# Kernel optimization log

Hardware: AMD Instinct MI355X
Metric: run time of the kernel (lower is better)

Reference implementation:

```python
import jax, jax.numpy as jnp
import numpy as np

B, S, DM, H = 2, 4096, 512, 8
DEPTH = DM // H


def setup_inputs() -> dict:
    key = jax.random.key(0)
    ks = jax.random.split(key, 12)
    scale = 1.0 / np.sqrt(DM)
    return {
        "q": jax.random.normal(ks[0], (B, S, DM), jnp.float32),
        "k": jax.random.normal(ks[1], (B, S, DM), jnp.float32),
        "v": jax.random.normal(ks[2], (B, S, DM), jnp.float32),
        # padding-style mask: 1.0 = masked position, 0.0 = attend
        "mask": jax.random.bernoulli(ks[3], 0.1, (B, 1, 1, S)).astype(jnp.float32),
        "Wq": jax.random.normal(ks[4], (DM, DM), jnp.float32) * scale,
        "bq": jnp.zeros((DM,), jnp.float32),
        "Wk": jax.random.normal(ks[5], (DM, DM), jnp.float32) * scale,
        "bk": jnp.zeros((DM,), jnp.float32),
        "Wv": jax.random.normal(ks[6], (DM, DM), jnp.float32) * scale,
        "bv": jnp.zeros((DM,), jnp.float32),
        "Wo": jax.random.normal(ks[7], (DM, DM), jnp.float32) * scale,
        "bo": jnp.zeros((DM,), jnp.float32),
    }


def _split_heads(x):
    # [B, S, DM] -> [B, H, S, DEPTH]
    b, s, _ = x.shape
    return x.reshape(b, s, H, DEPTH).transpose(0, 2, 1, 3)


def reference(q, k, v, mask, Wq, bq, Wk, bk, Wv, bv, Wo, bo):
    qh = _split_heads(q @ Wq + bq)   # [B,H,S,D]
    kh = _split_heads(k @ Wk + bk)
    vh = _split_heads(v @ Wv + bv)
    logits = jnp.einsum("bhqd,bhkd->bhqk", qh, kh) / jnp.sqrt(
        jnp.asarray(DEPTH, qh.dtype))
    logits = logits + mask * (-1e9)
    attn = jax.nn.softmax(logits, axis=-1)          # [B,H,Sq,Sk]
    out = jnp.einsum("bhqk,bhkd->bhqd", attn, vh)   # [B,H,S,D]
    out = out.transpose(0, 2, 1, 3).reshape(q.shape[0], -1, DM)
    return out @ Wo + bo
```

## Files before the change

### kernel.cpp

```cpp
#include <hip/hip_runtime.h>
#include <math.h>

#define BDIM 2
#define SDIM 4096
#define DMODEL 512
#define NHEAD 8
#define DHEAD 64
#define MROWS (BDIM * SDIM)

typedef __attribute__((ext_vector_type(8))) short short8;
typedef __attribute__((ext_vector_type(4))) float f32x4;

#define MFMA16(a, b, c) __builtin_amdgcn_mfma_f32_16x16x32_bf16((a), (b), (c), 0, 0, 0)
#define EXP2F(x) __builtin_amdgcn_exp2f(x)

#define SCALE2 0.18033688011112042f
#define MASKMUL -1.442695040e9f
#define M0C 16.0f

__device__ inline void bf16_split(float x, short& h, short& l) {
  unsigned u = __float_as_uint(x);
  h = (short)(u >> 16);
  float hf = __uint_as_float(u & 0xffff0000u);
  l = (short)(__float_as_uint(x - hf) >> 16);
}

__global__ __launch_bounds__(256) void wsplit_kernel(
    const float* __restrict__ W0, const float* __restrict__ W1,
    const float* __restrict__ W2, const float* __restrict__ W3,
    short* __restrict__ T0h, short* __restrict__ T0l, short* __restrict__ T1h,
    short* __restrict__ T1l, short* __restrict__ T2h, short* __restrict__ T2l,
    short* __restrict__ T3h, short* __restrict__ T3l) {
  __shared__ short Th[64 * 72], Tl[64 * 72];
  const int tid = threadIdx.x;
  const int k0 = blockIdx.x * 64;
  const int n0 = blockIdx.y * 64;
  const int z = blockIdx.z;
  const float* W = (z == 0) ? W0 : (z == 1) ? W1 : (z == 2) ? W2 : W3;
  short* Oh = (z == 0) ? T0h : (z == 1) ? T1h : (z == 2) ? T2h : T3h;
  short* Ol = (z == 0) ? T0l : (z == 1) ? T1l : (z == 2) ? T2l : T3l;

  {
    const int r = tid >> 2;
    const int c16 = (tid & 3) * 16;
    short8 h0, h1, l0, l1;
#pragma unroll
    for (int g = 0; g < 2; g++) {
      const f32x4 a = *(const f32x4*)(W + (size_t)(k0 + r) * DMODEL + n0 + c16 + g * 8);
      const f32x4 b = *(const f32x4*)(W + (size_t)(k0 + r) * DMODEL + n0 + c16 + g * 8 + 4);
      short8& hh = g ? h1 : h0;
      short8& ll = g ? l1 : l0;
#pragma unroll
      for (int j = 0; j < 4; j++) {
        short x, y;
        bf16_split(a[j], x, y);
        hh[j] = x;
        ll[j] = y;
        bf16_split(b[j], x, y);
        hh[4 + j] = x;
        ll[4 + j] = y;
      }
    }
    *(short8*)&Th[r * 72 + c16] = h0;
    *(short8*)&Th[r * 72 + c16 + 8] = h1;
    *(short8*)&Tl[r * 72 + c16] = l0;
    *(short8*)&Tl[r * 72 + c16 + 8] = l1;
  }
  __syncthreads();
  {
    const int n = tid >> 2;
    const int kc = (tid & 3) * 16;
    short8 h0, h1, l0, l1;
#pragma unroll
    for (int i = 0; i < 8; i++) {
      h0[i] = Th[(kc + i) * 72 + n];
      h1[i] = Th[(kc + 8 + i) * 72 + n];
      l0[i] = Tl[(kc + i) * 72 + n];
      l1[i] = Tl[(kc + 8 + i) * 72 + n];
    }
    short* dh = Oh + (size_t)(n0 + n) * DMODEL + k0 + kc;
    short* dl = Ol + (size_t)(n0 + n) * DMODEL + k0 + kc;
    *(short8*)dh = h0;
    *(short8*)(dh + 8) = h1;
    *(short8*)dl = l0;
    *(short8*)(dl + 8) = l1;
  }
}

template <int MODE>
__global__ __launch_bounds__(256, 4) void proj_mfma_kernel(
    const float* __restrict__ X, const short* __restrict__ Wth,
    const short* __restrict__ Wtl, const float* __restrict__ bias,
    float* __restrict__ out, short* __restrict__ oh, short* __restrict__ ol) {
  __shared__ short Xh[64 * 72], Xl[64 * 72];
  __shared__ short Wh[64 * 72], Wl[64 * 72];

  const int tid = threadIdx.x;
  const int lane = tid & 63;
  const int w = tid >> 6;
  const int lane15 = lane & 15;
  const int quad = lane >> 4;
  const int wm = (w >> 1) * 32;
  const int wn = (w & 1) * 32;
  const int m0 = blockIdx.x * 64;
  const int n0 = blockIdx.y * 64;

  f32x4 c[2][2];
#pragma unroll
  for (int mt = 0; mt < 2; mt++)
#pragma unroll
    for (int nt = 0; nt < 2; nt++) c[mt][nt] = (f32x4){0.f, 0.f, 0.f, 0.f};

  const int sr = tid >> 2;
  const int sc16 = (tid & 3) * 16;

  for (int k0 = 0; k0 < DMODEL; k0 += 64) {
    {
      short8 h0, h1, l0, l1;
#pragma unroll
      for (int g = 0; g < 2; g++) {
        const f32x4 a =
            *(const f32x4*)(X + (size_t)(m0 + sr) * DMODEL + k0 + sc16 + g * 8);
        const f32x4 b = *(const f32x4*)(X + (size_t)(m0 + sr) * DMODEL + k0 +
                                        sc16 + g * 8 + 4);
        short8& hh = g ? h1 : h0;
        short8& ll = g ? l1 : l0;
#pragma unroll
        for (int j = 0; j < 4; j++) {
          short x, y;
          bf16_split(a[j], x, y);
          hh[j] = x;
          ll[j] = y;
          bf16_split(b[j], x, y);
          hh[4 + j] = x;
          ll[4 + j] = y;
        }
      }
      *(short8*)&Xh[sr * 72 + sc16] = h0;
      *(short8*)&Xh[sr * 72 + sc16 + 8] = h1;
      *(short8*)&Xl[sr * 72 + sc16] = l0;
      *(short8*)&Xl[sr * 72 + sc16 + 8] = l1;

      const short* wsh = Wth + (size_t)(n0 + sr) * DMODEL + k0 + sc16;
      const short* wsl = Wtl + (size_t)(n0 + sr) * DMODEL + k0 + sc16;
      *(short8*)&Wh[sr * 72 + sc16] = *(const short8*)wsh;
      *(short8*)&Wh[sr * 72 + sc16 + 8] = *(const short8*)(wsh + 8);
      *(short8*)&Wl[sr * 72 + sc16] = *(const short8*)wsl;
      *(short8*)&Wl[sr * 72 + sc16 + 8] = *(const short8*)(wsl + 8);
    }
    __syncthreads();

#pragma unroll
    for (int ks = 0; ks < 2; ks++) {
      short8 ah[2], al[2], bh[2], bl[2];
#pragma unroll
      for (int mt = 0; mt < 2; mt++) {
        const int xo = (wm + mt * 16 + lane15) * 72 + ks * 32 + quad * 8;
        ah[mt] = *(const short8*)&Xh[xo];
        al[mt] = *(const short8*)&Xl[xo];
      }
#pragma unroll
      for (int nt = 0; nt < 2; nt++) {
        const int wo = (wn + nt * 16 + lane15) * 72 + ks * 32 + quad * 8;
        bh[nt] = *(const short8*)&Wh[wo];
        bl[nt] = *(const short8*)&Wl[wo];
      }
#pragma unroll
      for (int mt = 0; mt < 2; mt++)
#pragma unroll
        for (int nt = 0; nt < 2; nt++) {
          c[mt][nt] = MFMA16(ah[mt], bh[nt], c[mt][nt]);
          c[mt][nt] = MFMA16(ah[mt], bl[nt], c[mt][nt]);
          c[mt][nt] = MFMA16(al[mt], bh[nt], c[mt][nt]);
        }
    }
    __syncthreads();
  }

#pragma unroll
  for (int nt = 0; nt < 2; nt++) {
    const int n = n0 + wn + nt * 16 + lane15;
    const float bb = bias[n];
#pragma unroll
    for (int mt = 0; mt < 2; mt++)
#pragma unroll
      for (int r = 0; r < 4; r++) {
        const int m = m0 + wm + mt * 16 + quad * 4 + r;
        const float val = c[mt][nt][r] + bb;
        if (MODE == 1) {
          const int bidx = m >> 12;
          const int s = m & 4095;
          const int hh = n >> 6;
          const int d = n & 63;
          const size_t off =
              ((size_t)(bidx * NHEAD + hh) * SDIM + s) * DHEAD + d;
          short x, y;
          bf16_split(val, x, y);
          oh[off] = x;
          ol[off] = y;
        } else {
          out[(size_t)m * DMODEL + n] = val;
        }
      }
  }
}

__global__ __launch_bounds__(256) void vtrans_kernel(
    const short* __restrict__ vh, const short* __restrict__ vl,
    short* __restrict__ vth, short* __restrict__ vtl) {
  __shared__ short Th[64 * 72], Tl[64 * 72];
  const int tid = threadIdx.x;
  const int s0 = blockIdx.x * 64;
  const int h = blockIdx.y;
  const int b = blockIdx.z;
  const size_t base = (size_t)(b * NHEAD + h) * SDIM * DHEAD;

  {
    const int s = tid >> 2;
    const int c = tid & 3;
    const short* srcH = vh + base + (size_t)(s0 + s) * DHEAD + c * 16;
    const short* srcL = vl + base + (size_t)(s0 + s) * DHEAD + c * 16;
    *(short8*)&Th[s * 72 + c * 16] = *(const short8*)srcH;
    *(short8*)&Th[s * 72 + c * 16 + 8] = *(const short8*)(srcH + 8);
    *(short8*)&Tl[s * 72 + c * 16] = *(const short8*)srcL;
    *(short8*)&Tl[s * 72 + c * 16 + 8] = *(const short8*)(srcL + 8);
  }
  __syncthreads();
  {
    const int d = tid & 63;
    const int cw = tid >> 6;
    short8 a0, a1, b0, b1;
#pragma unroll
    for (int i = 0; i < 8; i++) {
      a0[i] = Th[(cw * 16 + i) * 72 + d];
      a1[i] = Th[(cw * 16 + 8 + i) * 72 + d];
      b0[i] = Tl[(cw * 16 + i) * 72 + d];
      b1[i] = Tl[(cw * 16 + 8 + i) * 72 + d];
    }
    short* dstH = vth + base + (size_t)d * SDIM + s0 + cw * 16;
    short* dstL = vtl + base + (size_t)d * SDIM + s0 + cw * 16;
    *(short8*)dstH = a0;
    *(short8*)(dstH + 8) = a1;
    *(short8*)dstL = b0;
    *(short8*)(dstL + 8) = b1;
  }
}

#define KP 72
#define VP 72
#define PP 68

__global__ __launch_bounds__(256, 2) void flash_attn_kernel(
    const short* __restrict__ qhh, const short* __restrict__ qhl,
    const short* __restrict__ khh, const short* __restrict__ khl,
    const short* __restrict__ vth, const short* __restrict__ vtl,
    const float* __restrict__ mask, float* __restrict__ ctx) {
  __shared__ short Ksh[64 * KP], Ksl[64 * KP];
  __shared__ short Vsh[64 * VP], Vsl[64 * VP];
  __shared__ float Ps[128 * PP];

  const int tid = threadIdx.x;
  const int lane = tid & 63;
  const int w = tid >> 6;
  const int lane15 = lane & 15;
  const int quad = lane >> 4;
  const int q0 = blockIdx.x * 128;
  const int h = blockIdx.y;
  const int b = blockIdx.z;

  const size_t base = (size_t)(b * NHEAD + h) * SDIM * DHEAD;
  const short* Qh = qhh + base;
  const short* Ql = qhl + base;
  const short* Kh = khh + base;
  const short* Kl = khl + base;
  const short* Vh = vth + base;
  const short* Vl = vtl + base;
  const float* mb = mask + (size_t)b * SDIM;

  short8 qfh[2][2], qfl[2][2];
#pragma unroll
  for (int mt = 0; mt < 2; mt++) {
    const size_t row = q0 + w * 32 + mt * 16 + lane15;
#pragma unroll
    for (int ks = 0; ks < 2; ks++) {
      qfh[mt][ks] = *(const short8*)(Qh + row * DHEAD + ks * 32 + quad * 8);
      qfl[mt][ks] = *(const short8*)(Ql + row * DHEAD + ks * 32 + quad * 8);
    }
  }

  f32x4 o[2][4];
#pragma unroll
  for (int mt = 0; mt < 2; mt++)
#pragma unroll
    for (int dt = 0; dt < 4; dt++) o[mt][dt] = (f32x4){0.f, 0.f, 0.f, 0.f};
  float lr[2][4];
#pragma unroll
  for (int mt = 0; mt < 2; mt++)
#pragma unroll
    for (int r = 0; r < 4; r++) lr[mt][r] = 0.f;

  short8 onesb;
#pragma unroll
  for (int j = 0; j < 8; j++) onesb[j] = (short)0x3F80;

  const int sr = tid >> 2;
  const int sc = (tid & 3) * 16;

  for (int kt = 0; kt < SDIM / 64; kt++) {
    const int k0 = kt * 64;
    {
      const short8 a0 = *(const short8*)(Kh + (size_t)(k0 + sr) * DHEAD + sc);
      const short8 a1 = *(const short8*)(Kh + (size_t)(k0 + sr) * DHEAD + sc + 8);
      const short8 b0 = *(const short8*)(Kl + (size_t)(k0 + sr) * DHEAD + sc);
      const short8 b1 = *(const short8*)(Kl + (size_t)(k0 + sr) * DHEAD + sc + 8);
      const short8 c0 = *(const short8*)(Vh + (size_t)sr * SDIM + k0 + sc);
      const short8 c1 = *(const short8*)(Vh + (size_t)sr * SDIM + k0 + sc + 8);
      const short8 d0 = *(const short8*)(Vl + (size_t)sr * SDIM + k0 + sc);
      const short8 d1 = *(const short8*)(Vl + (size_t)sr * SDIM + k0 + sc + 8);
      *(short8*)&Ksh[sr * KP + sc] = a0;
      *(short8*)&Ksh[sr * KP + sc + 8] = a1;
      *(short8*)&Ksl[sr * KP + sc] = b0;
      *(short8*)&Ksl[sr * KP + sc + 8] = b1;
      *(short8*)&Vsh[sr * VP + sc] = c0;
      *(short8*)&Vsh[sr * VP + sc + 8] = c1;
      *(short8*)&Vsl[sr * VP + sc] = d0;
      *(short8*)&Vsl[sr * VP + sc + 8] = d1;
    }
    float mv[4];
#pragma unroll
    for (int nt = 0; nt < 4; nt++)
      mv[nt] = fmaf(mb[k0 + nt * 16 + lane15], MASKMUL, -M0C);
    __syncthreads();

#pragma unroll
    for (int mt = 0; mt < 2; mt++)
#pragma unroll
      for (int nt = 0; nt < 4; nt++) {
        f32x4 acc = (f32x4){0.f, 0.f, 0.f, 0.f};
#pragma unroll
        for (int ks = 0; ks < 2; ks++) {
          const int koff = (nt * 16 + lane15) * KP + ks * 32 + quad * 8;
          const short8 kbh = *(const short8*)&Ksh[koff];
          const short8 kbl = *(const short8*)&Ksl[koff];
          acc = MFMA16(qfh[mt][ks], kbh, acc);
          acc = MFMA16(qfh[mt][ks], kbl, acc);
          acc = MFMA16(qfl[mt][ks], kbh, acc);
        }
#pragma unroll
        for (int r = 0; r < 4; r++) {
          const float p = EXP2F(fmaf(acc[r], SCALE2, mv[nt]));
          Ps[(w * 32 + mt * 16 + quad * 4 + r) * PP + nt * 16 + lane15] = p;
        }
      }

    short8 pah[2][2], pal[2][2];
#pragma unroll
    for (int mt = 0; mt < 2; mt++)
#pragma unroll
      for (int kf = 0; kf < 2; kf++) {
        const float* pr =
            &Ps[(w * 32 + mt * 16 + lane15) * PP + kf * 32 + quad * 8];
        const f32x4 p0 = *(const f32x4*)pr;
        const f32x4 p1 = *(const f32x4*)(pr + 4);
        short8 ph, pl;
#pragma unroll
        for (int j = 0; j < 4; j++) {
          short hh, ll;
          bf16_split(p0[j], hh, ll);
          ph[j] = hh;
          pl[j] = ll;
        }
#pragma unroll
        for (int j = 0; j < 4; j++) {
          short hh, ll;
          bf16_split(p1[j], hh, ll);
          ph[4 + j] = hh;
          pl[4 + j] = ll;
        }
        pah[mt][kf] = ph;
        pal[mt][kf] = pl;
      }

#pragma unroll
    for (int mt = 0; mt < 2; mt++) {
      f32x4 racc = (f32x4){0.f, 0.f, 0.f, 0.f};
#pragma unroll
      for (int kf = 0; kf < 2; kf++) {
        racc = MFMA16(pah[mt][kf], onesb, racc);
        racc = MFMA16(pal[mt][kf], onesb, racc);
      }
#pragma unroll
      for (int r = 0; r < 4; r++) lr[mt][r] += racc[r];
    }

#pragma unroll
    for (int dt = 0; dt < 4; dt++)
#pragma unroll
      for (int kf = 0; kf < 2; kf++) {
        const int voff = (dt * 16 + lane15) * VP + kf * 32 + quad * 8;
        const short8 vbh = *(const short8*)&Vsh[voff];
        const short8 vbl = *(const short8*)&Vsl[voff];
#pragma unroll
        for (int mt = 0; mt < 2; mt++) {
          o[mt][dt] = MFMA16(pah[mt][kf], vbh, o[mt][dt]);
          o[mt][dt] = MFMA16(pah[mt][kf], vbl, o[mt][dt]);
          o[mt][dt] = MFMA16(pal[mt][kf], vbh, o[mt][dt]);
        }
      }
    __syncthreads();
  }

  float inv[2][4];
#pragma unroll
  for (int mt = 0; mt < 2; mt++)
#pragma unroll
    for (int r = 0; r < 4; r++) inv[mt][r] = 1.f / lr[mt][r];
#pragma unroll
  for (int mt = 0; mt < 2; mt++)
#pragma unroll
    for (int dt = 0; dt < 4; dt++)
#pragma unroll
      for (int r = 0; r < 4; r++) {
        const int q = q0 + w * 32 + mt * 16 + quad * 4 + r;
        const int col = h * DHEAD + dt * 16 + lane15;
        ctx[((size_t)b * SDIM + q) * DMODEL + col] = o[mt][dt][r] * inv[mt][r];
      }
}

extern "C" void kernel_launch(void* const* d_in, const int* in_sizes, int n_in,
                              void* d_out, int out_size, void* d_ws,
                              size_t ws_size, hipStream_t stream) {
  const float* q = (const float*)d_in[0];
  const float* k = (const float*)d_in[1];
  const float* v = (const float*)d_in[2];
  const float* mask = (const float*)d_in[3];
  const float* Wq = (const float*)d_in[4];
  const float* bq = (const float*)d_in[5];
  const float* Wk = (const float*)d_in[6];
  const float* bk = (const float*)d_in[7];
  const float* Wv = (const float*)d_in[8];
  const float* bv = (const float*)d_in[9];
  const float* Wo = (const float*)d_in[10];
  const float* bo = (const float*)d_in[11];
  float* out = (float*)d_out;

  char* W = (char*)d_ws;
  const size_t SZB = (size_t)MROWS * DMODEL * sizeof(short);
  short* q_h = (short*)(W + 0 * SZB);
  short* q_l = (short*)(W + 1 * SZB);
  short* k_h = (short*)(W + 2 * SZB);
  short* k_l = (short*)(W + 3 * SZB);
  short* v_h = (short*)(W + 4 * SZB);
  short* v_l = (short*)(W + 5 * SZB);
  short* vt_h = (short*)(W + 6 * SZB);
  short* vt_l = (short*)(W + 7 * SZB);
  float* ctx = (float*)(W + 4 * SZB);
  const size_t WSZ = (size_t)DMODEL * DMODEL * sizeof(short);
  char* WT = W + 8 * SZB;
  short* wtq_h = (short*)(WT + 0 * WSZ);
  short* wtq_l = (short*)(WT + 1 * WSZ);
  short* wtk_h = (short*)(WT + 2 * WSZ);
  short* wtk_l = (short*)(WT + 3 * WSZ);
  short* wtv_h = (short*)(WT + 4 * WSZ);
  short* wtv_l = (short*)(WT + 5 * WSZ);
  short* wto_h = (short*)(WT + 6 * WSZ);
  short* wto_l = (short*)(WT + 7 * WSZ);

  wsplit_kernel<<<dim3(DMODEL / 64, DMODEL / 64, 4), 256, 0, stream>>>(
      Wq, Wk, Wv, Wo, wtq_h, wtq_l, wtk_h, wtk_l, wtv_h, wtv_l, wto_h, wto_l);

  const dim3 gproj(MROWS / 64, DMODEL / 64);
  proj_mfma_kernel<1><<<gproj, 256, 0, stream>>>(q, wtq_h, wtq_l, bq, nullptr,
                                                 q_h, q_l);
  proj_mfma_kernel<1><<<gproj, 256, 0, stream>>>(k, wtk_h, wtk_l, bk, nullptr,
                                                 k_h, k_l);
  proj_mfma_kernel<1><<<gproj, 256, 0, stream>>>(v, wtv_h, wtv_l, bv, nullptr,
                                                 v_h, v_l);

  vtrans_kernel<<<dim3(SDIM / 64, NHEAD, BDIM), 256, 0, stream>>>(v_h, v_l,
                                                                  vt_h, vt_l);

  flash_attn_kernel<<<dim3(SDIM / 128, NHEAD, BDIM), 256, 0, stream>>>(
      q_h, q_l, k_h, k_l, vt_h, vt_l, mask, ctx);

  proj_mfma_kernel<0><<<gproj, 256, 0, stream>>>(ctx, wto_h, wto_l, bo, out,
                                                 nullptr, nullptr);
}
```

Measured before the change: 424.5 us.

## Pre-split activations, double-buffer projection GEMM with LDS DMA, prefetch K/V in attention

```diff
diff --git a/kernel.cpp b/kernel.cpp
--- a/kernel.cpp
+++ b/kernel.cpp
@@ -17,6 +17,11 @@
 #define SCALE2 0.18033688011112042f
 #define MASKMUL -1.442695040e9f
 #define M0C 16.0f
+
+#define GLOAD_LDS16(g, l)                                                     \
+  __builtin_amdgcn_global_load_lds(                                           \
+      (const __attribute__((address_space(1))) void*)(g),                     \
+      (__attribute__((address_space(3))) void*)(l), 16, 0, 0)
 
 __device__ inline void bf16_split(float x, short& h, short& l) {
   unsigned u = __float_as_uint(x);
@@ -87,98 +92,110 @@
   }
 }
 
+__global__ __launch_bounds__(256) void xsplit_kernel(const float* __restrict__ X,
+                                                     short* __restrict__ Xh,
+                                                     short* __restrict__ Xl) {
+  const size_t i = ((size_t)blockIdx.x * 256 + threadIdx.x) * 8;
+  const f32x4 a = *(const f32x4*)(X + i);
+  const f32x4 b = *(const f32x4*)(X + i + 4);
+  short8 h, l;
+#pragma unroll
+  for (int j = 0; j < 4; j++) {
+    short x, y;
+    bf16_split(a[j], x, y);
+    h[j] = x;
+    l[j] = y;
+    bf16_split(b[j], x, y);
+    h[4 + j] = x;
+    l[4 + j] = y;
+  }
+  *(short8*)(Xh + i) = h;
+  *(short8*)(Xl + i) = l;
+}
+
 template <int MODE>
-__global__ __launch_bounds__(256, 4) void proj_mfma_kernel(
-    const float* __restrict__ X, const short* __restrict__ Wth,
-    const short* __restrict__ Wtl, const float* __restrict__ bias,
-    float* __restrict__ out, short* __restrict__ oh, short* __restrict__ ol) {
-  __shared__ short Xh[64 * 72], Xl[64 * 72];
-  __shared__ short Wh[64 * 72], Wl[64 * 72];
-
+__global__ __launch_bounds__(512, 2) void proj2_kernel(
+    const short* __restrict__ Xh, const short* __restrict__ Xl,
+    const short* __restrict__ Wth, const short* __restrict__ Wtl,
+    const float* __restrict__ bias, float* __restrict__ out,
+    short* __restrict__ oh, short* __restrict__ ol) {
+  __shared__ short L[2 * 20480];
   const int tid = threadIdx.x;
   const int lane = tid & 63;
   const int w = tid >> 6;
   const int lane15 = lane & 15;
   const int quad = lane >> 4;
-  const int wm = (w >> 1) * 32;
-  const int wn = (w & 1) * 32;
   const int m0 = blockIdx.x * 64;
-  const int n0 = blockIdx.y * 64;
-
-  f32x4 c[2][2];
+  const int n0 = blockIdx.y * 256;
+  const int wm = (w >> 2) * 32;
+  const int wn = (w & 3) * 64;
+
+  const short* gp[5];
+  int ldso[5];
+#pragma unroll
+  for (int i = 0; i < 5; i++) {
+    const int idx = w * 5 + i;
+    const int g = idx * 64 + lane;
+    if (g < 512) {
+      const short* src = (g < 256) ? Xh : Xl;
+      const int a = g & 255;
+      gp[i] = src + (size_t)(m0 + (a >> 2)) * DMODEL + (a & 3) * 8;
+    } else {
+      const int gg = g - 512;
+      const short* src = (gg < 1024) ? Wth : Wtl;
+      const int a = gg & 1023;
+      gp[i] = src + (size_t)(n0 + (a >> 2)) * DMODEL + (a & 3) * 8;
+    }
+    ldso[i] = idx * 512;
+  }
+
+  f32x4 c[2][4];
 #pragma unroll
   for (int mt = 0; mt < 2; mt++)
 #pragma unroll
-    for (int nt = 0; nt < 2; nt++) c[mt][nt] = (f32x4){0.f, 0.f, 0.f, 0.f};
-
-  const int sr = tid >> 2;
-  const int sc16 = (tid & 3) * 16;
-
-  for (int k0 = 0; k0 < DMODEL; k0 += 64) {
-    {
-      short8 h0, h1, l0, l1;
-#pragma unroll
-      for (int g = 0; g < 2; g++) {
-        const f32x4 a =
-            *(const f32x4*)(X + (size_t)(m0 + sr) * DMODEL + k0 + sc16 + g * 8);
-        const f32x4 b = *(const f32x4*)(X + (size_t)(m0 + sr) * DMODEL + k0 +
-                                        sc16 + g * 8 + 4);
-        short8& hh = g ? h1 : h0;
-        short8& ll = g ? l1 : l0;
-#pragma unroll
-        for (int j = 0; j < 4; j++) {
-          short x, y;
-          bf16_split(a[j], x, y);
-          hh[j] = x;
-          ll[j] = y;
-          bf16_split(b[j], x, y);
-          hh[4 + j] = x;
-          ll[4 + j] = y;
-        }
-      }
-      *(short8*)&Xh[sr * 72 + sc16] = h0;
-      *(short8*)&Xh[sr * 72 + sc16 + 8] = h1;
-      *(short8*)&Xl[sr * 72 + sc16] = l0;
-      *(short8*)&Xl[sr * 72 + sc16 + 8] = l1;
-
-      const short* wsh = Wth + (size_t)(n0 + sr) * DMODEL + k0 + sc16;
-      const short* wsl = Wtl + (size_t)(n0 + sr) * DMODEL + k0 + sc16;
-      *(short8*)&Wh[sr * 72 + sc16] = *(const short8*)wsh;
-      *(short8*)&Wh[sr * 72 + sc16 + 8] = *(const short8*)(wsh + 8);
-      *(short8*)&Wl[sr * 72 + sc16] = *(const short8*)wsl;
-      *(short8*)&Wl[sr * 72 + sc16 + 8] = *(const short8*)(wsl + 8);
-    }
+    for (int nt = 0; nt < 4; nt++) c[mt][nt] = (f32x4){0.f, 0.f, 0.f, 0.f};
+
+  constexpr int NT = DMODEL / 32;
+
+#pragma unroll
+  for (int i = 0; i < 5; i++) GLOAD_LDS16(gp[i], &L[ldso[i]]);
+
+  for (int t = 0; t < NT; t++) {
     __syncthreads();
-
-#pragma unroll
-    for (int ks = 0; ks < 2; ks++) {
-      short8 ah[2], al[2], bh[2], bl[2];
-#pragma unroll
-      for (int mt = 0; mt < 2; mt++) {
-        const int xo = (wm + mt * 16 + lane15) * 72 + ks * 32 + quad * 8;
-        ah[mt] = *(const short8*)&Xh[xo];
-        al[mt] = *(const short8*)&Xl[xo];
-      }
-#pragma unroll
-      for (int nt = 0; nt < 2; nt++) {
-        const int wo = (wn + nt * 16 + lane15) * 72 + ks * 32 + quad * 8;
-        bh[nt] = *(const short8*)&Wh[wo];
-        bl[nt] = *(const short8*)&Wl[wo];
-      }
-#pragma unroll
-      for (int mt = 0; mt < 2; mt++)
-#pragma unroll
-        for (int nt = 0; nt < 2; nt++) {
-          c[mt][nt] = MFMA16(ah[mt], bh[nt], c[mt][nt]);
-          c[mt][nt] = MFMA16(ah[mt], bl[nt], c[mt][nt]);
-          c[mt][nt] = MFMA16(al[mt], bh[nt], c[mt][nt]);
-        }
-    }
-    __syncthreads();
-  }
-
-#pragma unroll
-  for (int nt = 0; nt < 2; nt++) {
+    if (t + 1 < NT) {
+      short* dst = &L[((t + 1) & 1) * 20480];
+#pragma unroll
+      for (int i = 0; i < 5; i++)
+        GLOAD_LDS16(gp[i] + (t + 1) * 32, dst + ldso[i]);
+    }
+    const short* buf = &L[(t & 1) * 20480];
+    short8 ah[2], al[2], bh[4], bl[4];
+#pragma unroll
+    for (int mt = 0; mt < 2; mt++) {
+      const int r = wm + mt * 16 + lane15;
+      ah[mt] = *(const short8*)&buf[r * 32 + quad * 8];
+      al[mt] = *(const short8*)&buf[2048 + r * 32 + quad * 8];
+    }
+#pragma unroll
+    for (int nt = 0; nt < 4; nt++) {
+      const int r = wn + nt * 16 + lane15;
+      bh[nt] = *(const short8*)&buf[4096 + r * 32 + quad * 8];
+      bl[nt] = *(const short8*)&buf[12288 + r * 32 + quad * 8];
+    }
+    __builtin_amdgcn_s_setprio(1);
+#pragma unroll
+    for (int mt = 0; mt < 2; mt++)
+#pragma unroll
+      for (int nt = 0; nt < 4; nt++) {
+        c[mt][nt] = MFMA16(ah[mt], bh[nt], c[mt][nt]);
+        c[mt][nt] = MFMA16(ah[mt], bl[nt], c[mt][nt]);
+        c[mt][nt] = MFMA16(al[mt], bh[nt], c[mt][nt]);
+      }
+    __builtin_amdgcn_s_setprio(0);
+  }
+
+#pragma unroll
+  for (int nt = 0; nt < 4; nt++) {
     const int n = n0 + wn + nt * 16 + lane15;
     const float bb = bias[n];
 #pragma unroll
@@ -254,7 +271,8 @@
     const short* __restrict__ qhh, const short* __restrict__ qhl,
     const short* __restrict__ khh, const short* __restrict__ khl,
     const short* __restrict__ vth, const short* __restrict__ vtl,
-    const float* __restrict__ mask, float* __restrict__ ctx) {
+    const float* __restrict__ mask, short* __restrict__ ctxh,
+    short* __restrict__ ctxl) {
   __shared__ short Ksh[64 * KP], Ksl[64 * KP];
   __shared__ short Vsh[64 * VP], Vsl[64 * VP];
   __shared__ float Ps[128 * PP];
@@ -306,32 +324,48 @@
   const int sr = tid >> 2;
   const int sc = (tid & 3) * 16;
 
+  short8 rg[8];
+  rg[0] = *(const short8*)(Kh + (size_t)sr * DHEAD + sc);
+  rg[1] = *(const short8*)(Kh + (size_t)sr * DHEAD + sc + 8);
+  rg[2] = *(const short8*)(Kl + (size_t)sr * DHEAD + sc);
+  rg[3] = *(const short8*)(Kl + (size_t)sr * DHEAD + sc + 8);
+  rg[4] = *(const short8*)(Vh + (size_t)sr * SDIM + sc);
+  rg[5] = *(const short8*)(Vh + (size_t)sr * SDIM + sc + 8);
+  rg[6] = *(const short8*)(Vl + (size_t)sr * SDIM + sc);
+  rg[7] = *(const short8*)(Vl + (size_t)sr * SDIM + sc + 8);
+
   for (int kt = 0; kt < SDIM / 64; kt++) {
     const int k0 = kt * 64;
-    {
-      const short8 a0 = *(const short8*)(Kh + (size_t)(k0 + sr) * DHEAD + sc);
-      const short8 a1 = *(const short8*)(Kh + (size_t)(k0 + sr) * DHEAD + sc + 8);
-      const short8 b0 = *(const short8*)(Kl + (size_t)(k0 + sr) * DHEAD + sc);
-      const short8 b1 = *(const short8*)(Kl + (size_t)(k0 + sr) * DHEAD + sc + 8);
-      const short8 c0 = *(const short8*)(Vh + (size_t)sr * SDIM + k0 + sc);
-      const short8 c1 = *(const short8*)(Vh + (size_t)sr * SDIM + k0 + sc + 8);
-      const short8 d0 = *(const short8*)(Vl + (size_t)sr * SDIM + k0 + sc);
-      const short8 d1 = *(const short8*)(Vl + (size_t)sr * SDIM + k0 + sc + 8);
-      *(short8*)&Ksh[sr * KP + sc] = a0;
-      *(short8*)&Ksh[sr * KP + sc + 8] = a1;
-      *(short8*)&Ksl[sr * KP + sc] = b0;
-      *(short8*)&Ksl[sr * KP + sc + 8] = b1;
-      *(short8*)&Vsh[sr * VP + sc] = c0;
-      *(short8*)&Vsh[sr * VP + sc + 8] = c1;
-      *(short8*)&Vsl[sr * VP + sc] = d0;
-      *(short8*)&Vsl[sr * VP + sc + 8] = d1;
+    __builtin_amdgcn_s_barrier();
+    __builtin_amdgcn_sched_barrier(0);
+    *(short8*)&Ksh[sr * KP + sc] = rg[0];
+    *(short8*)&Ksh[sr * KP + sc + 8] = rg[1];
+    *(short8*)&Ksl[sr * KP + sc] = rg[2];
+    *(short8*)&Ksl[sr * KP + sc + 8] = rg[3];
+    *(short8*)&Vsh[sr * VP + sc] = rg[4];
+    *(short8*)&Vsh[sr * VP + sc + 8] = rg[5];
+    *(short8*)&Vsl[sr * VP + sc] = rg[6];
+    *(short8*)&Vsl[sr * VP + sc + 8] = rg[7];
+    if (kt + 1 < SDIM / 64) {
+      const int k1 = k0 + 64;
+      rg[0] = *(const short8*)(Kh + (size_t)(k1 + sr) * DHEAD + sc);
+      rg[1] = *(const short8*)(Kh + (size_t)(k1 + sr) * DHEAD + sc + 8);
+      rg[2] = *(const short8*)(Kl + (size_t)(k1 + sr) * DHEAD + sc);
+      rg[3] = *(const short8*)(Kl + (size_t)(k1 + sr) * DHEAD + sc + 8);
+      rg[4] = *(const short8*)(Vh + (size_t)sr * SDIM + k1 + sc);
+      rg[5] = *(const short8*)(Vh + (size_t)sr * SDIM + k1 + sc + 8);
+      rg[6] = *(const short8*)(Vl + (size_t)sr * SDIM + k1 + sc);
+      rg[7] = *(const short8*)(Vl + (size_t)sr * SDIM + k1 + sc + 8);
     }
     float mv[4];
 #pragma unroll
     for (int nt = 0; nt < 4; nt++)
       mv[nt] = fmaf(mb[k0 + nt * 16 + lane15], MASKMUL, -M0C);
-    __syncthreads();
-
+    asm volatile("s_waitcnt lgkmcnt(0)" ::: "memory");
+    __builtin_amdgcn_s_barrier();
+    __builtin_amdgcn_sched_barrier(0);
+
+    __builtin_amdgcn_s_setprio(1);
 #pragma unroll
     for (int mt = 0; mt < 2; mt++)
 #pragma unroll
@@ -352,6 +386,7 @@
           Ps[(w * 32 + mt * 16 + quad * 4 + r) * PP + nt * 16 + lane15] = p;
         }
       }
+    __builtin_amdgcn_s_setprio(0);
 
     short8 pah[2][2], pal[2][2];
 #pragma unroll
@@ -381,6 +416,7 @@
         pal[mt][kf] = pl;
       }
 
+    __builtin_amdgcn_s_setprio(1);
 #pragma unroll
     for (int mt = 0; mt < 2; mt++) {
       f32x4 racc = (f32x4){0.f, 0.f, 0.f, 0.f};
@@ -407,7 +443,7 @@
           o[mt][dt] = MFMA16(pal[mt][kf], vbh, o[mt][dt]);
         }
       }
-    __syncthreads();
+    __builtin_amdgcn_s_setprio(0);
   }
 
   float inv[2][4];
@@ -423,7 +459,12 @@
       for (int r = 0; r < 4; r++) {
         const int q = q0 + w * 32 + mt * 16 + quad * 4 + r;
         const int col = h * DHEAD + dt * 16 + lane15;
-        ctx[((size_t)b * SDIM + q) * DMODEL + col] = o[mt][dt][r] * inv[mt][r];
+        const float val = o[mt][dt][r] * inv[mt][r];
+        short x, y;
+        bf16_split(val, x, y);
+        const size_t off = ((size_t)b * SDIM + q) * DMODEL + col;
+        ctxh[off] = x;
+        ctxl[off] = y;
       }
 }
 
@@ -454,9 +495,10 @@
   short* v_l = (short*)(W + 5 * SZB);
   short* vt_h = (short*)(W + 6 * SZB);
   short* vt_l = (short*)(W + 7 * SZB);
-  float* ctx = (float*)(W + 4 * SZB);
+  short* cx_h = (short*)(W + 8 * SZB);
+  short* cx_l = (short*)(W + 9 * SZB);
   const size_t WSZ = (size_t)DMODEL * DMODEL * sizeof(short);
-  char* WT = W + 8 * SZB;
+  char* WT = W + 10 * SZB;
   short* wtq_h = (short*)(WT + 0 * WSZ);
   short* wtq_l = (short*)(WT + 1 * WSZ);
   short* wtk_h = (short*)(WT + 2 * WSZ);
@@ -469,20 +511,25 @@
   wsplit_kernel<<<dim3(DMODEL / 64, DMODEL / 64, 4), 256, 0, stream>>>(
       Wq, Wk, Wv, Wo, wtq_h, wtq_l, wtk_h, wtk_l, wtv_h, wtv_l, wto_h, wto_l);
 
-  const dim3 gproj(MROWS / 64, DMODEL / 64);
-  proj_mfma_kernel<1><<<gproj, 256, 0, stream>>>(q, wtq_h, wtq_l, bq, nullptr,
-                                                 q_h, q_l);
-  proj_mfma_kernel<1><<<gproj, 256, 0, stream>>>(k, wtk_h, wtk_l, bk, nullptr,
-                                                 k_h, k_l);
-  proj_mfma_kernel<1><<<gproj, 256, 0, stream>>>(v, wtv_h, wtv_l, bv, nullptr,
-                                                 v_h, v_l);
+  const dim3 gx(MROWS * DMODEL / (256 * 8));
+  const dim3 gp2(MROWS / 64, DMODEL / 256);
+
+  xsplit_kernel<<<gx, 256, 0, stream>>>(q, cx_h, cx_l);
+  proj2_kernel<1><<<gp2, 512, 0, stream>>>(cx_h, cx_l, wtq_h, wtq_l, bq,
+                                           nullptr, q_h, q_l);
+  xsplit_kernel<<<gx, 256, 0, stream>>>(k, cx_h, cx_l);
+  proj2_kernel<1><<<gp2, 512, 0, stream>>>(cx_h, cx_l, wtk_h, wtk_l, bk,
+                                           nullptr, k_h, k_l);
+  xsplit_kernel<<<gx, 256, 0, stream>>>(v, cx_h, cx_l);
+  proj2_kernel<1><<<gp2, 512, 0, stream>>>(cx_h, cx_l, wtv_h, wtv_l, bv,
+                                           nullptr, v_h, v_l);
 
   vtrans_kernel<<<dim3(SDIM / 64, NHEAD, BDIM), 256, 0, stream>>>(v_h, v_l,
                                                                   vt_h, vt_l);
 
   flash_attn_kernel<<<dim3(SDIM / 128, NHEAD, BDIM), 256, 0, stream>>>(
-      q_h, q_l, k_h, k_l, vt_h, vt_l, mask, ctx);
-
-  proj_mfma_kernel<0><<<gproj, 256, 0, stream>>>(ctx, wto_h, wto_l, bo, out,
-                                                 nullptr, nullptr);
-}
+      q_h, q_l, k_h, k_l, vt_h, vt_l, mask, cx_h, cx_l);
+
+  proj2_kernel<0><<<gp2, 512, 0, stream>>>(cx_h, cx_l, wto_h, wto_l, bo, out,
+                                           nullptr, nullptr);
+}
```

New measurement: 415.3 us. 2.2% less time.
